# Optimization experiments

Measured on AMD Instinct MI355X. Metric: run time of the kernel, lower is better.

## Reference

```python
import jax, jax.numpy as jnp
import numpy as np
import math

D_MODEL = 512
D_STATE = 16
D_CONV = 4
EXPAND = 2
D_INNER = EXPAND * D_MODEL
DT_RANK = math.ceil(D_MODEL / 16)
B_SZ, L_SEQ = 4, 4096


def setup_inputs() -> dict:
    key = jax.random.key(0)
    ks = jax.random.split(key, 32)
    f32 = jnp.float32

    def nrm(k, shape, s=0.02):
        return (jax.random.normal(k, shape, dtype=f32) * s)

    # dt bias init (inverse softplus of dt in [dt_min, dt_max])
    def dt_bias(k):
        u = jax.random.uniform(k, (D_INNER,), dtype=f32)
        dt = jnp.exp(u * (math.log(0.1) - math.log(1e-3)) + math.log(1e-3))
        dt = jnp.clip(dt, 1e-4, None)
        return dt + jnp.log(-jnp.expm1(-dt))

    Alog = jnp.log(jnp.broadcast_to(jnp.arange(1, D_STATE + 1, dtype=f32), (D_INNER, D_STATE)))
    dt_std = DT_RANK ** (-0.5)

    inp = {
        'hidden_states': jax.random.normal(ks[0], (B_SZ, L_SEQ, D_MODEL), dtype=f32),
        'another_hidden_states': jax.random.normal(ks[1], (B_SZ, L_SEQ, D_MODEL), dtype=f32),
        'in_proj_w': nrm(ks[2], (2 * D_INNER, D_MODEL)),
        'in_proj_g_w': nrm(ks[3], (2 * D_INNER, D_MODEL)),
        'convw_f': nrm(ks[4], (D_INNER, D_CONV), 0.1),
        'convb_f': jnp.zeros((D_INNER,), f32),
        'convw_r': nrm(ks[5], (D_INNER, D_CONV), 0.1),
        'convb_r': jnp.zeros((D_INNER,), f32),
        'convw_g': nrm(ks[6], (D_INNER, D_CONV), 0.1),
        'convb_g': jnp.zeros((D_INNER,), f32),
        'xproj_f': nrm(ks[7], (DT_RANK + 2 * D_STATE, D_INNER)),
        'xproj_r': nrm(ks[8], (DT_RANK + 2 * D_STATE, D_INNER)),
        'xproj_g': nrm(ks[9], (DT_RANK + 2 * D_STATE, D_INNER)),
        'dtw_f': jax.random.uniform(ks[10], (D_INNER, DT_RANK), minval=-dt_std, maxval=dt_std, dtype=f32),
        'dtb_f': dt_bias(ks[11]),
        'dtw_r': jax.random.uniform(ks[12], (D_INNER, DT_RANK), minval=-dt_std, maxval=dt_std, dtype=f32),
        'dtb_r': dt_bias(ks[13]),
        'dtw_g': jax.random.uniform(ks[14], (D_INNER, DT_RANK), minval=-dt_std, maxval=dt_std, dtype=f32),
        'dtb_g': dt_bias(ks[15]),
        'Alog_f': Alog, 'Alog_r': Alog, 'Alog_g': Alog,
        'D_f': jnp.ones((D_INNER,), f32),
        'D_r': jnp.ones((D_INNER,), f32),
        'D_g': jnp.ones((D_INNER,), f32),
        'out_proj_w': nrm(ks[16], (D_MODEL, D_INNER)),
    }
    return inp


def _branch(xz, convw, convb, xproj, dtw, dtb, Alog, Dp):
    # xz: (B, L, 2*d_inner)
    b, l, _ = xz.shape
    d = xz.shape[-1] // 2
    x, z = xz[..., :d], xz[..., d:]
    # causal depthwise conv1d over L (pad left d_conv-1), then SiLU
    xc = jnp.transpose(x, (0, 2, 1))  # (B, d, L)
    xc = jax.lax.conv_general_dilated(
        xc, convw[:, None, :], (1,), [(convw.shape[-1] - 1, 0)],
        dimension_numbers=('NCH', 'OIH', 'NCH'), feature_group_count=d)
    xc = xc + convb[None, :, None]
    x = jax.nn.silu(jnp.transpose(xc, (0, 2, 1)))  # (B, L, d)
    # input-dependent dt, B, C
    dbl = x @ xproj.T  # (B, L, dt_rank + 2n)
    r = dtw.shape[1]
    n = Alog.shape[1]
    dt = jax.nn.softplus(dbl[..., :r] @ dtw.T + dtb)  # (B, L, d)
    Bs = dbl[..., r:r + n]   # (B, L, n)
    Cs = dbl[..., r + n:]    # (B, L, n)
    A = -jnp.exp(Alog)       # (d, n)

    def step(h, inp):
        dt_t, x_t, B_t, C_t = inp  # (B,d),(B,d),(B,n),(B,n)
        h = jnp.exp(dt_t[:, :, None] * A) * h + (dt_t * x_t)[:, :, None] * B_t[:, None, :]
        y = jnp.einsum('bdn,bn->bd', h, C_t)
        return h, y

    h0 = jnp.zeros((b, d, n), dtype=x.dtype)
    xs = (jnp.swapaxes(dt, 0, 1), jnp.swapaxes(x, 0, 1),
          jnp.swapaxes(Bs, 0, 1), jnp.swapaxes(Cs, 0, 1))
    _, ys = jax.lax.scan(step, h0, xs)
    y = jnp.swapaxes(ys, 0, 1) + Dp * x  # (B, L, d)
    return y * jax.nn.silu(z)


def reference(hidden_states, another_hidden_states, in_proj_w, in_proj_g_w,
              convw_f, convb_f, convw_r, convb_r, convw_g, convb_g,
              xproj_f, xproj_r, xproj_g,
              dtw_f, dtb_f, dtw_r, dtb_r, dtw_g, dtb_g,
              Alog_f, Alog_r, Alog_g, D_f, D_r, D_g, out_proj_w):
    xz = hidden_states @ in_proj_w.T           # (B, L, 2*d_inner)
    axz = another_hidden_states @ in_proj_g_w.T
    y_f = _branch(xz, convw_f, convb_f, xproj_f, dtw_f, dtb_f, Alog_f, D_f)
    y_r = jnp.flip(_branch(jnp.flip(xz, axis=1), convw_r, convb_r, xproj_r, dtw_r, dtb_r, Alog_r, D_r), axis=1)
    y_g = _branch(axz, convw_g, convb_g, xproj_g, dtw_g, dtb_g, Alog_g, D_g)
    out = ((y_f + y_r) * jax.nn.silu(y_g)) @ out_proj_w.T  # (B, L, d_model)
    return out
```

## Files before the change

kernel.cpp:

```cpp
#include <hip/hip_runtime.h>
#include <hip/hip_bf16.h>
#include <math.h>

#define L_SEQ 4096
#define B_SZ 4
#define D_MODEL 512
#define D_INNER 1024
#define DT_RANK 32
#define D_STATE 16
#define M_ROWS (B_SZ * L_SEQ)
#define NC 64
#define CHK (L_SEQ / NC)

typedef __hip_bfloat16 bf16;
typedef __bf16 bf16x8 __attribute__((ext_vector_type(8)));
typedef float f32x4 __attribute__((ext_vector_type(4)));
struct us8 { ushort4 a, b; };

__device__ __forceinline__ unsigned short f2us(float f) {
    union { bf16 h; unsigned short u; } t;
    t.h = __float2bfloat16(f);
    return t.u;
}
__device__ __forceinline__ float us2f(unsigned short u) {
    union { bf16 h; unsigned short u; } t;
    t.u = u;
    return __bfloat162float(t.h);
}

__device__ __forceinline__ float silu_f(float x) {
    const float xc = fminf(fmaxf(x, -60.0f), 60.0f);
    return x / (1.0f + __expf(-xc));
}
__device__ __forceinline__ float softplus_f(float x) {
    if (x > 20.0f) return x;
    if (x < -20.0f) return __expf(x);
    return log1pf(__expf(x));
}

struct CvtArgs {
    const float* src[9];
    unsigned short* dst[9];
    unsigned int vend[9];
    int nseg;
};
__global__ __launch_bounds__(256)
void cvt_multi(CvtArgs a)
{
    const unsigned int v = blockIdx.x * 256 + threadIdx.x;
    if (v >= a.vend[a.nseg - 1]) return;
    int s = 0;
    unsigned int vstart = 0;
    while (v >= a.vend[s]) { vstart = a.vend[s]; ++s; }
    const size_t lv = (size_t)(v - vstart) * 4;
    const float4 f = *(const float4*)(a.src[s] + lv);
    ushort4 o;
    o.x = f2us(f.x); o.y = f2us(f.y); o.z = f2us(f.z); o.w = f2us(f.w);
    *(ushort4*)(a.dst[s] + lv) = o;
}

template<int BM, int BN, int BK, int WY, int WX, int GATED, int EPI, int CT>
__global__ __launch_bounds__(256)
void gemm_mfma(const unsigned short* __restrict__ A,
               const unsigned short* __restrict__ A2,
               const unsigned short* __restrict__ W,
               const float* __restrict__ bias,
               void* __restrict__ Cp, unsigned short* __restrict__ C2p,
               int K, int lda, int ldb, int ldc)
{
    constexpr int CPR = BK / 8;
    constexpr int SWM = CPR - 1;
    constexpr int RPW = 64 / CPR;
    constexpr int NPA = BM / (4 * RPW);
    constexpr int NPB = BN / (4 * RPW);
    constexpr int WGX = BN / (WX * 16);
    static_assert(WGX * (BM / (WY * 16)) == 4, "4 waves");
    __shared__ unsigned short As[BM * BK];
    __shared__ unsigned short Bs[BN * BK];

    const int tid  = threadIdx.x;
    const int lane = tid & 63;
    const int wave = tid >> 6;
    const int wx = wave % WGX, wy = wave / WGX;
    const int l15 = lane & 15, quad = lane >> 4;
    const long row0 = (long)blockIdx.y * BM;
    const long col0 = (long)blockIdx.x * BN;

    const int rin = lane / CPR;
    const int gc  = (lane % CPR) ^ (rin & SWM);

    f32x4 acc[WY][WX];
#pragma unroll
    for (int i = 0; i < WY; ++i)
#pragma unroll
        for (int j = 0; j < WX; ++j) acc[i][j] = (f32x4){0.f, 0.f, 0.f, 0.f};

    for (int k0 = 0; k0 < K; k0 += BK) {
        if (GATED == 0) {
#pragma unroll
            for (int p = 0; p < NPA; ++p) {
                const int rb = (p * 4 + wave) * RPW;
                const unsigned short* gp = A + (row0 + rb + rin) * (long)lda + k0 + gc * 8;
                const int lb = __builtin_amdgcn_readfirstlane(rb * BK);
                __builtin_amdgcn_global_load_lds(
                    (const __attribute__((address_space(1))) void*)gp,
                    (__attribute__((address_space(3))) void*)(As + lb), 16, 0, 0);
            }
        } else {
#pragma unroll
            for (int v = 0; v < BM * BK / 2048; ++v) {
                const int e = (v * 256 + tid) * 8;
                const int r = e / BK, c = (e % BK) / 8;
                const long off = (row0 + r) * (long)lda + k0 + c * 8;
                const us8 ta = *(const us8*)(A + off);
                const us8 tg = *(const us8*)(A2 + off);
                us8 t;
                t.a.x = f2us(us2f(ta.a.x) * silu_f(us2f(tg.a.x)));
                t.a.y = f2us(us2f(ta.a.y) * silu_f(us2f(tg.a.y)));
                t.a.z = f2us(us2f(ta.a.z) * silu_f(us2f(tg.a.z)));
                t.a.w = f2us(us2f(ta.a.w) * silu_f(us2f(tg.a.w)));
                t.b.x = f2us(us2f(ta.b.x) * silu_f(us2f(tg.b.x)));
                t.b.y = f2us(us2f(ta.b.y) * silu_f(us2f(tg.b.y)));
                t.b.z = f2us(us2f(ta.b.z) * silu_f(us2f(tg.b.z)));
                t.b.w = f2us(us2f(ta.b.w) * silu_f(us2f(tg.b.w)));
                *(us8*)&As[r * BK + ((c ^ (r & SWM)) * 8)] = t;
            }
        }
#pragma unroll
        for (int p = 0; p < NPB; ++p) {
            const int rb = (p * 4 + wave) * RPW;
            const unsigned short* gp = W + (col0 + rb + rin) * (long)ldb + k0 + gc * 8;
            const int lb = __builtin_amdgcn_readfirstlane(rb * BK);
            __builtin_amdgcn_global_load_lds(
                (const __attribute__((address_space(1))) void*)gp,
                (__attribute__((address_space(3))) void*)(Bs + lb), 16, 0, 0);
        }
        __syncthreads();

#pragma unroll
        for (int kk = 0; kk < BK / 32; ++kk) {
            bf16x8 aF[WY], bF[WX];
#pragma unroll
            for (int i = 0; i < WY; ++i) {
                const int r  = wy * WY * 16 + i * 16 + l15;
                const int kc = (kk * 4 + quad) ^ (r & SWM);
                aF[i] = *(const bf16x8*)&As[r * BK + kc * 8];
            }
#pragma unroll
            for (int j = 0; j < WX; ++j) {
                const int r  = wx * WX * 16 + j * 16 + l15;
                const int kc = (kk * 4 + quad) ^ (r & SWM);
                bF[j] = *(const bf16x8*)&Bs[r * BK + kc * 8];
            }
#pragma unroll
            for (int i = 0; i < WY; ++i)
#pragma unroll
                for (int j = 0; j < WX; ++j)
                    acc[i][j] = __builtin_amdgcn_mfma_f32_16x16x32_bf16(
                        aF[i], bF[j], acc[i][j], 0, 0, 0);
        }
        __syncthreads();
    }

#pragma unroll
    for (int i = 0; i < WY; ++i)
#pragma unroll
        for (int j = 0; j < WX; ++j) {
            const long mb = row0 + wy * WY * 16 + i * 16 + quad * 4;
            const long n  = col0 + wx * WX * 16 + j * 16 + l15;
            const float bv = (EPI == 1) ? bias[n] : 0.0f;
#pragma unroll
            for (int r = 0; r < 4; ++r) {
                float val = acc[i][j][r];
                if (EPI == 1) val = softplus_f(val + bv);
                const long off = (mb + r) * (long)ldc + n;
                if (CT == 0) ((unsigned short*)Cp)[off] = f2us(val);
                else         ((float*)Cp)[off] = val;
                if (EPI == 2 && n < DT_RANK) C2p[(mb + r) * DT_RANK + n] = f2us(val);
            }
        }
}

__global__ __launch_bounds__(256)
void conv_silu8(const unsigned short* __restrict__ xz, const float* __restrict__ w,
                const float* __restrict__ bias, unsigned short* __restrict__ xb, int rev)
{
    const int idx = blockIdx.x * 256 + threadIdx.x;
    const int g = idx & 127;
    const int m = idx >> 7;
    const int b = m >> 12;
    const int t = m & (L_SEQ - 1);
    const int d = g * 8;

    float s[8];
    {
        const float4 b0 = *(const float4*)(bias + d);
        const float4 b1 = *(const float4*)(bias + d + 4);
        s[0] = b0.x; s[1] = b0.y; s[2] = b0.z; s[3] = b0.w;
        s[4] = b1.x; s[5] = b1.y; s[6] = b1.z; s[7] = b1.w;
    }
    float4 wv[8];
#pragma unroll
    for (int j = 0; j < 8; ++j) wv[j] = *(const float4*)(w + (d + j) * 4);

    const unsigned short* xbase = xz + (size_t)b * L_SEQ * 2048 + d;
#pragma unroll
    for (int k = 0; k < 4; ++k) {
        const int src = t - 3 + k;
        if (src >= 0) {
            const int sm = rev ? (L_SEQ - 1 - src) : src;
            const us8 xv = *(const us8*)(xbase + (size_t)sm * 2048);
            const float tap[8] = {us2f(xv.a.x), us2f(xv.a.y), us2f(xv.a.z), us2f(xv.a.w),
                                  us2f(xv.b.x), us2f(xv.b.y), us2f(xv.b.z), us2f(xv.b.w)};
#pragma unroll
            for (int j = 0; j < 8; ++j) {
                const float wk = (k == 0) ? wv[j].x : (k == 1) ? wv[j].y
                               : (k == 2) ? wv[j].z : wv[j].w;
                s[j] = fmaf(wk, tap[j], s[j]);
            }
        }
    }
    us8 o;
    o.a.x = f2us(silu_f(s[0])); o.a.y = f2us(silu_f(s[1]));
    o.a.z = f2us(silu_f(s[2])); o.a.w = f2us(silu_f(s[3]));
    o.b.x = f2us(silu_f(s[4])); o.b.y = f2us(silu_f(s[5]));
    o.b.z = f2us(silu_f(s[6])); o.b.w = f2us(silu_f(s[7]));
    *(us8*)(xb + (size_t)m * 1024 + d) = o;
}

__device__ __forceinline__ bool a_struct_fast(const float* __restrict__ Alog,
                                              int d, float& A0)
{
    A0 = -__expf(Alog[d * 16]);
    bool fast = true;
#pragma unroll
    for (int n = 1; n < 16; ++n) {
        const float an = -__expf(Alog[d * 16 + n]);
        const float tg = (float)(n + 1) * A0;
        fast = fast && (fabsf(an - tg) <= 1e-5f * fabsf(tg));
    }
    return fast;
}
__device__ __forceinline__ void pow_tree16(float e1, float w[16])
{
    w[0] = e1;
    w[1] = w[0] * w[0];  w[2] = w[1] * w[0];  w[3] = w[1] * w[1];
    w[4] = w[3] * w[0];  w[5] = w[3] * w[1];  w[6] = w[3] * w[2];  w[7] = w[3] * w[3];
#pragma unroll
    for (int n = 8; n < 16; ++n) w[n] = w[7] * w[n - 8];
}

__global__ __launch_bounds__(1024)
void scan_a(const unsigned short* __restrict__ dtq, const unsigned short* __restrict__ xq,
            const float* __restrict__ dbl, const float* __restrict__ Alog,
            float* __restrict__ hF, float* __restrict__ Ssum)
{
    const int d = threadIdx.x;
    const int c = blockIdx.x;
    const int b = blockIdx.y;

    __shared__ float Bsh[CHK][16];
    {
        const int tl = d >> 4, nl = d & 15;
        Bsh[tl][nl] = dbl[((size_t)b * L_SEQ + c * CHK + tl) * 64 + DT_RANK + nl];
    }
    __syncthreads();

    float A0;
    const bool fast = a_struct_fast(Alog, d, A0);

    float h[16];
#pragma unroll
    for (int n = 0; n < 16; ++n) h[n] = 0.0f;
    float S = 0.0f;

    const size_t base = ((size_t)b * L_SEQ + c * CHK) * 1024 + d;
    const unsigned short* dtp = dtq + base;
    const unsigned short* xp  = xq + base;

    if (fast) {
        unsigned short bd[4], bx[4];
#pragma unroll
        for (int i = 0; i < 4; ++i) {
            bd[i] = dtp[(size_t)i * 1024];
            bx[i] = xp[(size_t)i * 1024];
        }
        for (int t0 = 0; t0 < CHK; t0 += 4) {
            unsigned short nd[4], nx[4];
            const bool pf = (t0 + 4 < CHK);
            if (pf) {
#pragma unroll
                for (int i = 0; i < 4; ++i) {
                    nd[i] = dtp[(size_t)(t0 + 4 + i) * 1024];
                    nx[i] = xp[(size_t)(t0 + 4 + i) * 1024];
                }
            }
#pragma unroll
            for (int i = 0; i < 4; ++i) {
                const float dt = us2f(bd[i]);
                const float xv = us2f(bx[i]);
                S += dt;
                const float dtx = dt * xv;
                float w[16];
                pow_tree16(__expf(dt * A0), w);
#pragma unroll
                for (int n = 0; n < 16; ++n)
                    h[n] = fmaf(w[n], h[n], dtx * Bsh[t0 + i][n]);
            }
            if (pf) {
#pragma unroll
                for (int i = 0; i < 4; ++i) { bd[i] = nd[i]; bx[i] = nx[i]; }
            }
        }
    } else {
        float Acoef[16];
#pragma unroll
        for (int n = 0; n < 16; ++n) Acoef[n] = -__expf(Alog[d * 16 + n]);
        unsigned short vd = dtp[0], vx = xp[0];
        for (int t = 0; t < CHK; ++t) {
            unsigned short vd2 = 0, vx2 = 0;
            if (t + 1 < CHK) {
                vd2 = dtp[(size_t)(t + 1) * 1024];
                vx2 = xp[(size_t)(t + 1) * 1024];
            }
            const float dt = us2f(vd);
            const float xv = us2f(vx);
            S += dt;
            const float dtx = dt * xv;
#pragma unroll
            for (int n = 0; n < 16; ++n)
                h[n] = fmaf(__expf(dt * Acoef[n]), h[n], dtx * Bsh[t][n]);
            vd = vd2; vx = vx2;
        }
    }

    float* hp = hF + (((size_t)(b * NC + c) * 1024 + d) << 4);
#pragma unroll
    for (int n = 0; n < 16; ++n) hp[n] = h[n];
    Ssum[(size_t)(b * NC + c) * 1024 + d] = S;
}

__global__ __launch_bounds__(256)
void scan_b(float* __restrict__ hF, const float* __restrict__ Ssum,
            const float* __restrict__ Alog)
{
    const int idx = blockIdx.x * 256 + threadIdx.x;
    const int n  = idx & 15;
    const int dn = idx >> 4;
    const int d  = dn & (D_INNER - 1);
    const int b  = dn >> 10;

    const float Acoef = -__expf(Alog[d * 16 + n]);
    float H = 0.0f;
    for (int c = 0; c < NC; ++c) {
        const size_t base = (size_t)(b * NC + c) * 1024 + d;
        const float S = Ssum[base];
        float* hp = hF + (base << 4) + n;
        const float hOld = *hp;
        *hp = H;
        H = fmaf(__expf(Acoef * S), H, hOld);
    }
}

__global__ __launch_bounds__(1024)
void scan_c(const unsigned short* __restrict__ dtq, const unsigned short* __restrict__ xq,
            const float* __restrict__ dbl, const float* __restrict__ hF,
            const float* __restrict__ Alog, const float* __restrict__ Dp,
            const unsigned short* __restrict__ xz, unsigned short* __restrict__ yout,
            int rev, int acc)
{
    const int d = threadIdx.x;
    const int c = blockIdx.x;
    const int b = blockIdx.y;

    __shared__ float Bsh[CHK][16];
    __shared__ float Csh[CHK][16];
    {
        const int tl = d >> 4, nl = d & 15;
        const size_t rb = ((size_t)b * L_SEQ + c * CHK + tl) * 64;
        Bsh[tl][nl] = dbl[rb + DT_RANK + nl];
        Csh[tl][nl] = dbl[rb + DT_RANK + D_STATE + nl];
    }
    __syncthreads();

    float A0;
    const bool fast = a_struct_fast(Alog, d, A0);
    const float Dd = Dp[d];

    float h[16];
    {
        const float* hp = hF + (((size_t)(b * NC + c) * 1024 + d) << 4);
#pragma unroll
        for (int n = 0; n < 16; ++n) h[n] = hp[n];
    }

    const size_t base = ((size_t)b * L_SEQ + c * CHK) * 1024 + d;
    const unsigned short* dtp = dtq + base;
    const unsigned short* xp  = xq + base;
    const unsigned short* z_base = xz + (size_t)b * L_SEQ * 2048 + D_INNER + d;
    unsigned short* y_base = yout + (size_t)b * L_SEQ * D_INNER + d;

    if (fast) {
        unsigned short bd[4], bx[4], bz[4];
#pragma unroll
        for (int i = 0; i < 4; ++i) {
            bd[i] = dtp[(size_t)i * 1024];
            bx[i] = xp[(size_t)i * 1024];
            const int tg = c * CHK + i;
            const int tm = rev ? (L_SEQ - 1 - tg) : tg;
            bz[i] = z_base[(size_t)tm * 2048];
        }
        for (int t0 = 0; t0 < CHK; t0 += 4) {
            unsigned short nd[4], nx[4], nz[4];
            const bool pf = (t0 + 4 < CHK);
            if (pf) {
#pragma unroll
                for (int i = 0; i < 4; ++i) {
                    nd[i] = dtp[(size_t)(t0 + 4 + i) * 1024];
                    nx[i] = xp[(size_t)(t0 + 4 + i) * 1024];
                    const int tg = c * CHK + t0 + 4 + i;
                    const int tm = rev ? (L_SEQ - 1 - tg) : tg;
                    nz[i] = z_base[(size_t)tm * 2048];
                }
            }
#pragma unroll
            for (int i = 0; i < 4; ++i) {
                const float dt = us2f(bd[i]);
                const float xv = us2f(bx[i]);
                const float dtx = dt * xv;
                float w[16];
                pow_tree16(__expf(dt * A0), w);
                float y = 0.0f;
#pragma unroll
                for (int n = 0; n < 16; ++n) {
                    h[n] = fmaf(w[n], h[n], dtx * Bsh[t0 + i][n]);
                    y = fmaf(h[n], Csh[t0 + i][n], y);
                }
                const int tg = c * CHK + t0 + i;
                const int tm = rev ? (L_SEQ - 1 - tg) : tg;
                const float z = us2f(bz[i]);
                float yo = (y + Dd * xv) * silu_f(z);
                const size_t oi = (size_t)tm * D_INNER;
                if (acc) yo += us2f(y_base[oi]);
                y_base[oi] = f2us(yo);
            }
            if (pf) {
#pragma unroll
                for (int i = 0; i < 4; ++i) { bd[i] = nd[i]; bx[i] = nx[i]; bz[i] = nz[i]; }
            }
        }
    } else {
        float Acoef[16];
#pragma unroll
        for (int n = 0; n < 16; ++n) Acoef[n] = -__expf(Alog[d * 16 + n]);
        unsigned short vd = dtp[0], vx = xp[0];
        for (int t = 0; t < CHK; ++t) {
            unsigned short vd2 = 0, vx2 = 0;
            if (t + 1 < CHK) {
                vd2 = dtp[(size_t)(t + 1) * 1024];
                vx2 = xp[(size_t)(t + 1) * 1024];
            }
            const float dt = us2f(vd);
            const float xv = us2f(vx);
            const float dtx = dt * xv;
            float y = 0.0f;
#pragma unroll
            for (int n = 0; n < 16; ++n) {
                h[n] = fmaf(__expf(dt * Acoef[n]), h[n], dtx * Bsh[t][n]);
                y = fmaf(h[n], Csh[t][n], y);
            }
            const int tg = c * CHK + t;
            const int tm = rev ? (L_SEQ - 1 - tg) : tg;
            const float z = us2f(z_base[(size_t)tm * 2048]);
            float yo = (y + Dd * xv) * silu_f(z);
            const size_t oi = (size_t)tm * D_INNER;
            if (acc) yo += us2f(y_base[oi]);
            y_base[oi] = f2us(yo);
            vd = vd2; vx = vx2;
        }
    }
}

extern "C" void kernel_launch(void* const* d_in, const int* in_sizes, int n_in,
                              void* d_out, int out_size, void* d_ws, size_t ws_size,
                              hipStream_t stream)
{
    const float* hs    = (const float*)d_in[0];
    const float* ahs   = (const float*)d_in[1];
    const float* in_w  = (const float*)d_in[2];
    const float* in_gw = (const float*)d_in[3];
    const float* convw[3] = {(const float*)d_in[4], (const float*)d_in[6], (const float*)d_in[8]};
    const float* convb[3] = {(const float*)d_in[5], (const float*)d_in[7], (const float*)d_in[9]};
    const float* xproj[3] = {(const float*)d_in[10], (const float*)d_in[11], (const float*)d_in[12]};
    const float* dtw[3]   = {(const float*)d_in[13], (const float*)d_in[15], (const float*)d_in[17]};
    const float* dtbias[3]= {(const float*)d_in[14], (const float*)d_in[16], (const float*)d_in[18]};
    const float* Alog[3]  = {(const float*)d_in[19], (const float*)d_in[20], (const float*)d_in[21]};
    const float* Dp[3]    = {(const float*)d_in[22], (const float*)d_in[23], (const float*)d_in[24]};
    const float* out_w = (const float*)d_in[25];

    unsigned short* regA = (unsigned short*)d_ws;
    float* dbl  = (float*)(regA + (size_t)M_ROWS * 2048);
    unsigned short* xb  = (unsigned short*)(dbl + (size_t)M_ROWS * 64);
    unsigned short* dtv = xb  + (size_t)M_ROWS * 1024;
    unsigned short* yfr = dtv + (size_t)M_ROWS * 1024;
    unsigned short* yg  = yfr + (size_t)M_ROWS * 1024;
    float* hF   = (float*)(yg + (size_t)M_ROWS * 1024);
    float* Ssum = hF + (size_t)B_SZ * NC * 1024 * 16;
    unsigned short* dtin = (unsigned short*)(Ssum + (size_t)B_SZ * NC * 1024);
    unsigned short* wbig = dtin + (size_t)M_ROWS * 32;
    unsigned short* wout = wbig + (size_t)2048 * 512;
    unsigned short* wxpb = wout + (size_t)512 * 1024;
    unsigned short* wdtb = wxpb + (size_t)3 * 64 * 1024;
    unsigned short* inb  = yfr;

    const dim3 blk(256);

    {
        CvtArgs a;
        unsigned int acc = 0;
        const float* srcs[9] = {ahs, in_gw, out_w, xproj[0], xproj[1], xproj[2],
                                dtw[0], dtw[1], dtw[2]};
        unsigned short* dsts[9] = {inb, wbig, wout,
                                   wxpb, wxpb + 64 * 1024, wxpb + 2 * 64 * 1024,
                                   wdtb, wdtb + 1024 * 32, wdtb + 2 * 1024 * 32};
        const unsigned int sz[9] = {M_ROWS * 512u, 2048u * 512u, 512u * 1024u,
                                    64u * 1024u, 64u * 1024u, 64u * 1024u,
                                    1024u * 32u, 1024u * 32u, 1024u * 32u};
        for (int i = 0; i < 9; ++i) {
            a.src[i] = srcs[i]; a.dst[i] = dsts[i];
            acc += sz[i] / 4; a.vend[i] = acc;
        }
        a.nseg = 9;
        cvt_multi<<<dim3((acc + 255) / 256), blk, 0, stream>>>(a);
    }

    const int order[3] = {2, 0, 1};

    gemm_mfma<128,128,64,4,4,0,0,0><<<dim3(16, 128), blk, 0, stream>>>(
        inb, nullptr, wbig, nullptr, regA, nullptr, D_MODEL, D_MODEL, D_MODEL, 2048);

    for (int oi = 0; oi < 3; ++oi) {
        const int br = order[oi];
        const int rev  = (br == 1) ? 1 : 0;
        const int accf = (br == 1) ? 1 : 0;
        unsigned short* ybuf = (br == 2) ? yg : yfr;

        if (br == 0) {
            CvtArgs a;
            a.src[0] = hs;   a.dst[0] = inb;  a.vend[0] = M_ROWS * 512u / 4;
            a.src[1] = in_w; a.dst[1] = wbig; a.vend[1] = a.vend[0] + 2048u * 512u / 4;
            a.nseg = 2;
            cvt_multi<<<dim3((a.vend[1] + 255) / 256), blk, 0, stream>>>(a);
            gemm_mfma<128,128,64,4,4,0,0,0><<<dim3(16, 128), blk, 0, stream>>>(
                inb, nullptr, wbig, nullptr, regA, nullptr, D_MODEL, D_MODEL, D_MODEL, 2048);
        }

        conv_silu8<<<dim3(M_ROWS * 128 / 256), blk, 0, stream>>>(
            regA, convw[br], convb[br], xb, rev);

        gemm_mfma<64,64,64,2,2,0,2,1><<<dim3(1, 256), blk, 0, stream>>>(
            xb, nullptr, wxpb + br * 64 * 1024, nullptr, dbl, dtin,
            D_INNER, D_INNER, D_INNER, 64);

        gemm_mfma<128,128,32,4,4,0,1,0><<<dim3(8, 128), blk, 0, stream>>>(
            dtin, nullptr, wdtb + br * 1024 * 32, dtbias[br], dtv, nullptr,
            DT_RANK, DT_RANK, DT_RANK, D_INNER);

        scan_a<<<dim3(NC, B_SZ), dim3(1024), 0, stream>>>(dtv, xb, dbl, Alog[br], hF, Ssum);
        scan_b<<<dim3((B_SZ * D_INNER * 16) / 256), blk, 0, stream>>>(hF, Ssum, Alog[br]);
        scan_c<<<dim3(NC, B_SZ), dim3(1024), 0, stream>>>(
            dtv, xb, dbl, hF, Alog[br], Dp[br], regA, ybuf, rev, accf);
    }

    gemm_mfma<128,128,64,4,4,1,0,1><<<dim3(4, 128), blk, 0, stream>>>(
        yfr, yg, wout, nullptr, d_out, nullptr, D_INNER, D_INNER, D_INNER, D_MODEL);
}
```

Measured before the change: 985.7 us.

## Fuse silu gate into reverse scan epilogue and remap GEMM workgroups across XCDs

The final reverse-branch scan now multiplies its accumulated y_f+y_r output by silu(y_g) before storing, so the output projection GEMM runs ungated and no longer reads and combines two activation tensors per A-tile load. The GEMM kernel also remaps linear block IDs so consecutive workgroups are spread across eight groups (XCD-style swizzle), aiming to improve L2 locality of shared tiles. This adds one extra bf16 load per element in the scan epilogue and changes rounding slightly because the gate is applied before the bf16 store.

```diff
diff --git a/kernel.cpp b/kernel.cpp
--- a/kernel.cpp
+++ b/kernel.cpp
@@ -83,8 +83,17 @@
     const int wave = tid >> 6;
     const int wx = wave % WGX, wy = wave / WGX;
     const int l15 = lane & 15, quad = lane >> 4;
-    const long row0 = (long)blockIdx.y * BM;
-    const long col0 = (long)blockIdx.x * BN;
+
+    const int nwg = gridDim.x * gridDim.y;
+    int bid = blockIdx.y * gridDim.x + blockIdx.x;
+    if ((nwg & 7) == 0) {
+        const int cpx = nwg >> 3;
+        bid = (bid & 7) * cpx + (bid >> 3);
+    }
+    const int bxi = bid % gridDim.x;
+    const int byi = bid / gridDim.x;
+    const long row0 = (long)byi * BM;
+    const long col0 = (long)bxi * BN;
 
     const int rin = lane / CPR;
     const int gc  = (lane % CPR) ^ (rin & SWM);
@@ -367,7 +376,7 @@
             const float* __restrict__ dbl, const float* __restrict__ hF,
             const float* __restrict__ Alog, const float* __restrict__ Dp,
             const unsigned short* __restrict__ xz, unsigned short* __restrict__ yout,
-            int rev, int acc)
+            const unsigned short* __restrict__ gate, int rev, int acc)
 {
     const int d = threadIdx.x;
     const int c = blockIdx.x;
@@ -398,10 +407,11 @@
     const unsigned short* dtp = dtq + base;
     const unsigned short* xp  = xq + base;
     const unsigned short* z_base = xz + (size_t)b * L_SEQ * 2048 + D_INNER + d;
+    const unsigned short* g_base = gate ? gate + (size_t)b * L_SEQ * D_INNER + d : nullptr;
     unsigned short* y_base = yout + (size_t)b * L_SEQ * D_INNER + d;
 
     if (fast) {
-        unsigned short bd[4], bx[4], bz[4];
+        unsigned short bd[4], bx[4], bz[4], bg[4];
 #pragma unroll
         for (int i = 0; i < 4; ++i) {
             bd[i] = dtp[(size_t)i * 1024];
@@ -409,9 +419,10 @@
             const int tg = c * CHK + i;
             const int tm = rev ? (L_SEQ - 1 - tg) : tg;
             bz[i] = z_base[(size_t)tm * 2048];
+            bg[i] = g_base ? g_base[(size_t)tm * D_INNER] : (unsigned short)0;
         }
         for (int t0 = 0; t0 < CHK; t0 += 4) {
-            unsigned short nd[4], nx[4], nz[4];
+            unsigned short nd[4], nx[4], nz[4], ng[4];
             const bool pf = (t0 + 4 < CHK);
             if (pf) {
 #pragma unroll
@@ -421,6 +432,7 @@
                     const int tg = c * CHK + t0 + 4 + i;
                     const int tm = rev ? (L_SEQ - 1 - tg) : tg;
                     nz[i] = z_base[(size_t)tm * 2048];
+                    ng[i] = g_base ? g_base[(size_t)tm * D_INNER] : (unsigned short)0;
                 }
             }
 #pragma unroll
@@ -442,11 +454,12 @@
                 float yo = (y + Dd * xv) * silu_f(z);
                 const size_t oi = (size_t)tm * D_INNER;
                 if (acc) yo += us2f(y_base[oi]);
+                if (g_base) yo *= silu_f(us2f(bg[i]));
                 y_base[oi] = f2us(yo);
             }
             if (pf) {
 #pragma unroll
-                for (int i = 0; i < 4; ++i) { bd[i] = nd[i]; bx[i] = nx[i]; bz[i] = nz[i]; }
+                for (int i = 0; i < 4; ++i) { bd[i] = nd[i]; bx[i] = nx[i]; bz[i] = nz[i]; bg[i] = ng[i]; }
             }
         }
     } else {
@@ -475,6 +488,7 @@
             float yo = (y + Dd * xv) * silu_f(z);
             const size_t oi = (size_t)tm * D_INNER;
             if (acc) yo += us2f(y_base[oi]);
+            if (g_base) yo *= silu_f(us2f(g_base[oi]));
             y_base[oi] = f2us(yo);
             vd = vd2; vx = vx2;
         }
@@ -544,6 +558,7 @@
         const int rev  = (br == 1) ? 1 : 0;
         const int accf = (br == 1) ? 1 : 0;
         unsigned short* ybuf = (br == 2) ? yg : yfr;
+        const unsigned short* gatep = (br == 1) ? yg : nullptr;
 
         if (br == 0) {
             CvtArgs a;
@@ -569,9 +584,9 @@
         scan_a<<<dim3(NC, B_SZ), dim3(1024), 0, stream>>>(dtv, xb, dbl, Alog[br], hF, Ssum);
         scan_b<<<dim3((B_SZ * D_INNER * 16) / 256), blk, 0, stream>>>(hF, Ssum, Alog[br]);
         scan_c<<<dim3(NC, B_SZ), dim3(1024), 0, stream>>>(
-            dtv, xb, dbl, hF, Alog[br], Dp[br], regA, ybuf, rev, accf);
-    }
-
-    gemm_mfma<128,128,64,4,4,1,0,1><<<dim3(4, 128), blk, 0, stream>>>(
-        yfr, yg, wout, nullptr, d_out, nullptr, D_INNER, D_INNER, D_INNER, D_MODEL);
-}
+            dtv, xb, dbl, hF, Alog[br], Dp[br], regA, ybuf, gatep, rev, accf);
+    }
+
+    gemm_mfma<128,128,64,4,4,0,0,1><<<dim3(4, 128), blk, 0, stream>>>(
+        yfr, nullptr, wout, nullptr, d_out, nullptr, D_INNER, D_INNER, D_INNER, D_MODEL);
+}
```

New measurement: 1.126 ms. 1.14x slower.
